# Kernel tuning notes

Measured on AMD Instinct MI355X. Metric: run time of the kernel, lower is better.

The kernel has to match this reference:

```python
import jax, jax.numpy as jnp
import numpy as np
import math

B, S, D, H, DQ, DV = 8, 1024, 1024, 16, 64, 64

def _layernorm(x, gamma, beta, eps=1e-5):
    mu = jnp.mean(x, axis=-1, keepdims=True)
    var = jnp.var(x, axis=-1, keepdims=True)
    return (x - mu) * jax.lax.rsqrt(var + eps) * gamma + beta

def setup_inputs() -> dict:
    key = jax.random.key(0)
    ks = jax.random.split(key, 6)
    x = jax.random.normal(ks[0], (B, S, D), dtype=jnp.float32)
    seq_lens = jax.random.randint(ks[1], (B,), 1, S + 1, dtype=jnp.int32)  # min 1 avoids fully-masked rows
    scale = 0.02
    Wq = jax.random.normal(ks[2], (D, H * DQ), dtype=jnp.float32) * scale
    Wkv = jax.random.normal(ks[3], (D, H * (DQ + DV)), dtype=jnp.float32) * scale
    Wo = jax.random.normal(ks[4], (H * DV, D), dtype=jnp.float32) * scale
    return {
        'x': x, 'seq_lens': seq_lens,
        'Wq': Wq, 'bq': jnp.zeros((H * DQ,), jnp.float32),
        'Wkv': Wkv, 'bkv': jnp.zeros((H * (DQ + DV),), jnp.float32),
        'Wo': Wo, 'bo': jnp.zeros((D,), jnp.float32),
        'gamma': jnp.ones((D,), jnp.float32), 'beta': jnp.zeros((D,), jnp.float32),
    }

def reference(x, seq_lens, Wq, bq, Wkv, bkv, Wo, bo, gamma, beta):
    # Decoder self-attention branch: query == key_value sequence.
    resid = x
    xn = _layernorm(x, gamma, beta)
    q = (xn @ Wq + bq).reshape(B, S, H, DQ).transpose(0, 2, 1, 3)      # bhqd
    kv = xn @ Wkv + bkv
    k = kv[..., : H * DQ].reshape(B, S, H, DQ).transpose(0, 2, 1, 3)   # bhkd
    v = kv[..., H * DQ :].reshape(B, S, H, DV).transpose(0, 2, 1, 3)   # bhkd
    scores = jnp.einsum('bhqd,bhkd->bhqk', q, k) / math.sqrt(DQ)
    key_pos = jnp.arange(S)
    pad_mask = key_pos[None, None, None, :] < seq_lens[:, None, None, None]  # [B,1,1,S]
    causal = jnp.tril(jnp.ones((S, S), dtype=bool))[None, None]              # [1,1,S,S]
    mask = pad_mask & causal
    scores = jnp.where(mask, scores, -jnp.inf)
    attn = jax.nn.softmax(scores, axis=-1)
    out = jnp.einsum('bhqk,bhkd->bhqd', attn, v)
    out = out.transpose(0, 2, 1, 3).reshape(B, S, H * DV)
    return out @ Wo + bo + resid
```

## Files before the change

### kernel.cpp

```cpp
#include <hip/hip_runtime.h>
#include <stdint.h>

#define ND 1024

typedef uint16_t u16;
typedef __bf16 bf16_t;
typedef bf16_t bf16x8 __attribute__((ext_vector_type(8)));
typedef float  f32x4  __attribute__((ext_vector_type(4)));
typedef u16    u16x8  __attribute__((ext_vector_type(8)));
typedef u16    u16x4  __attribute__((ext_vector_type(4)));

__device__ __forceinline__ float bf2f(u16 b){
    uint32_t u = ((uint32_t)b) << 16; float f; __builtin_memcpy(&f, &u, 4); return f;
}
__device__ __forceinline__ u16 f2bf(float f){
    uint32_t u; __builtin_memcpy(&u, &f, 4);
    u += 0x7FFFu + ((u >> 16) & 1u);
    return (u16)(u >> 16);
}
__device__ __forceinline__ bool bf_mode(const void* gamma){
    return *reinterpret_cast<const uint32_t*>(gamma) == 0x3F803F80u;
}
__device__ __forceinline__ float loadv(const void* p, int idx, bool bf){
    return bf ? bf2f(reinterpret_cast<const u16*>(p)[idx])
              : reinterpret_cast<const float*>(p)[idx];
}
__device__ __forceinline__ void gload16(const u16* g, u16* l){
    __builtin_amdgcn_global_load_lds(
        (const __attribute__((address_space(1))) void*)g,
        (__attribute__((address_space(3))) void*)l, 16, 0, 0);
}

__global__ __launch_bounds__(256) void k_ln(const void* __restrict__ x,
                                            const void* __restrict__ gamma,
                                            const void* __restrict__ beta,
                                            u16* __restrict__ xn){
    const bool bf = bf_mode(gamma);
    const int row = blockIdx.x;
    const int tid = threadIdx.x;
    const int base = row * ND + tid * 4;
    float v[4];
    if (bf){
        u16x4 t = *reinterpret_cast<const u16x4*>(reinterpret_cast<const u16*>(x) + base);
        #pragma unroll
        for (int e = 0; e < 4; e++) v[e] = bf2f(t[e]);
    } else {
        float4 t = *reinterpret_cast<const float4*>(reinterpret_cast<const float*>(x) + base);
        v[0] = t.x; v[1] = t.y; v[2] = t.z; v[3] = t.w;
    }
    float s1 = v[0] + v[1] + v[2] + v[3];
    float s2 = v[0]*v[0] + v[1]*v[1] + v[2]*v[2] + v[3]*v[3];
    #pragma unroll
    for (int off = 32; off; off >>= 1){
        s1 += __shfl_xor(s1, off);
        s2 += __shfl_xor(s2, off);
    }
    __shared__ float red1[4], red2[4];
    if ((tid & 63) == 0){ red1[tid >> 6] = s1; red2[tid >> 6] = s2; }
    __syncthreads();
    s1 = red1[0] + red1[1] + red1[2] + red1[3];
    s2 = red2[0] + red2[1] + red2[2] + red2[3];
    const float mu  = s1 * (1.0f / ND);
    const float var = s2 * (1.0f / ND) - mu * mu;
    const float rs  = rsqrtf(var + 1e-5f);
    u16x4 o;
    #pragma unroll
    for (int e = 0; e < 4; e++){
        float g = loadv(gamma, tid*4 + e, bf);
        float b = loadv(beta,  tid*4 + e, bf);
        o[e] = f2bf((v[e] - mu) * rs * g + b);
    }
    *reinterpret_cast<u16x4*>(xn + base) = o;
}

__global__ __launch_bounds__(256) void k_wt(const void* __restrict__ W,
                                            const void* __restrict__ gamma,
                                            u16* __restrict__ WT, int Ncols){
    const bool bf = bf_mode(gamma);
    __shared__ float tile[32][33];
    const int n0 = blockIdx.x * 32, k0 = blockIdx.y * 32;
    const int tx = threadIdx.x & 31, ty = threadIdx.x >> 5;
    #pragma unroll
    for (int r = 0; r < 4; r++){
        int kk = ty + r * 8;
        tile[kk][tx] = loadv(W, (k0 + kk) * Ncols + n0 + tx, bf);
    }
    __syncthreads();
    #pragma unroll
    for (int r = 0; r < 4; r++){
        int nn = ty + r * 8;
        WT[(size_t)(n0 + nn) * 1024 + k0 + tx] = f2bf(tile[tx][nn]);
    }
}

template<int MODE>
__global__ __launch_bounds__(256) void k_gemm(const u16* __restrict__ A,
                                              const u16* __restrict__ BT,
                                              const void* __restrict__ bias0,
                                              const void* __restrict__ bias1,
                                              const void* __restrict__ xres,
                                              const void* __restrict__ gamma,
                                              u16* __restrict__ Qo, u16* __restrict__ Ko,
                                              u16* __restrict__ Vo, float* __restrict__ outf){
    const bool bf = bf_mode(gamma);
    __shared__ u16 Al[128 * 64];
    __shared__ u16 Bl[128 * 64];
    const int bm = blockIdx.x & 63, bn = blockIdx.x >> 6;
    const int tid = threadIdx.x, lane = tid & 63, w = tid >> 6;
    const int wr = w >> 1, wc = w & 1;
    const int l15 = lane & 15, g = lane >> 4;
    const int xr = (l15 & 7) * 8;
    f32x4 acc[4][4];
    #pragma unroll
    for (int m = 0; m < 4; m++)
        #pragma unroll
        for (int n = 0; n < 4; n++) acc[m][n] = f32x4{0.f, 0.f, 0.f, 0.f};

    const u16* Ag = A  + (size_t)(bm * 128) * 1024;
    const u16* Bg = BT + (size_t)(bn * 128) * 1024;
    const int srow = tid >> 3, sslot = tid & 7;
    const int sswz = (sslot * 8) ^ ((srow & 7) * 8);

    for (int k0 = 0; k0 < 1024; k0 += 64){
        #pragma unroll
        for (int call = 0; call < 4; call++){
            const int row = srow + call * 32;
            const int c   = tid + call * 256;
            gload16(Ag + (size_t)row * 1024 + k0 + sswz, Al + c * 8);
            gload16(Bg + (size_t)row * 1024 + k0 + sswz, Bl + c * 8);
        }
        __syncthreads();
        #pragma unroll
        for (int kc = 0; kc < 2; kc++){
            bf16x8 af[4], bfr[4];
            #pragma unroll
            for (int m = 0; m < 4; m++){
                const int row = wr*64 + m*16 + l15;
                u16x8 t = *reinterpret_cast<const u16x8*>(&Al[row*64 + ((kc*32 + g*8) ^ xr)]);
                af[m] = __builtin_bit_cast(bf16x8, t);
            }
            #pragma unroll
            for (int n = 0; n < 4; n++){
                const int row = wc*64 + n*16 + l15;
                u16x8 t = *reinterpret_cast<const u16x8*>(&Bl[row*64 + ((kc*32 + g*8) ^ xr)]);
                bfr[n] = __builtin_bit_cast(bf16x8, t);
            }
            #pragma unroll
            for (int m = 0; m < 4; m++)
                #pragma unroll
                for (int n = 0; n < 4; n++)
                    acc[m][n] = __builtin_amdgcn_mfma_f32_16x16x32_bf16(af[m], bfr[n], acc[m][n], 0, 0, 0);
        }
        __syncthreads();
    }
    #pragma unroll
    for (int m = 0; m < 4; m++){
        const int grow = bm * 128 + wr * 64 + m * 16 + g * 4;
        #pragma unroll
        for (int n = 0; n < 4; n++){
            const int gcol = bn * 128 + wc * 64 + n * 16 + l15;
            #pragma unroll
            for (int r = 0; r < 4; r++){
                float val = acc[m][n][r];
                const int rr = grow + r;
                if (MODE == 0){
                    const int b = rr >> 10, s = rr & 1023;
                    if (gcol < 1024){
                        int h = gcol >> 6, d = gcol & 63;
                        val = (val + loadv(bias0, gcol, bf)) * 0.18033688011112042f;
                        Qo[((size_t)(b*16 + h) * 1024 + s) * 64 + d] = f2bf(val);
                    } else if (gcol < 2048){
                        int n2 = gcol - 1024, h = n2 >> 6, d = n2 & 63;
                        val += loadv(bias1, n2, bf);
                        Ko[((size_t)(b*16 + h) * 1024 + s) * 64 + d] = f2bf(val);
                    } else {
                        int n3 = gcol - 2048, h = n3 >> 6, d = n3 & 63;
                        val += loadv(bias1, gcol - 1024, bf);
                        Vo[((size_t)(b*16 + h) * 1024 + s) * 64 + d] = f2bf(val);
                    }
                } else {
                    val += loadv(bias0, gcol, bf);
                    val += loadv(xres, (int)((size_t)rr * 1024 + gcol), bf);
                    outf[(size_t)rr * 1024 + gcol] = val;
                }
            }
        }
    }
}

__global__ __launch_bounds__(64, 4) void k_attn(const u16* __restrict__ Q,
                                                const u16* __restrict__ K,
                                                const u16* __restrict__ V,
                                                const int* __restrict__ seq_lens,
                                                u16* __restrict__ AO){
    __shared__ u16 Kl0[32 * 64], Kl1[32 * 64];
    __shared__ u16 Vt[64 * 32];
    __shared__ u16 Pl[32 * 32];
    const int bid = blockIdx.x;
    const int qb = 31 - (bid >> 7);
    const int bh = bid & 127;
    const int b = bh >> 4, h = bh & 15;
    const int lane = threadIdx.x;
    const int l15 = lane & 15, g = lane >> 4;
    const int seqlen = seq_lens[b];
    const int nkt = (min(qb * 32 + 31, seqlen - 1) >> 5) + 1;
    const size_t kvbase = (size_t)bh * 1024;

    bf16x8 qa[2][2];
    #pragma unroll
    for (int m = 0; m < 2; m++)
        #pragma unroll
        for (int kc = 0; kc < 2; kc++){
            const u16* qp = Q + (kvbase + qb*32 + m*16 + l15) * 64 + kc*32 + g*8;
            qa[m][kc] = __builtin_bit_cast(bf16x8, *reinterpret_cast<const u16x8*>(qp));
        }

    float m_run[2] = {-3.0e38f, -3.0e38f};
    float l_run[2] = {0.f, 0.f};
    f32x4 oacc[2][4];
    #pragma unroll
    for (int m = 0; m < 2; m++)
        #pragma unroll
        for (int nf = 0; nf < 4; nf++) oacc[m][nf] = f32x4{0.f, 0.f, 0.f, 0.f};

    const int srow8 = lane >> 3, sslot = lane & 7;
    u16x8 vr[4];

    auto stageK = [&](int kt, u16* dst){
        #pragma unroll
        for (int call = 0; call < 4; call++){
            const int row = srow8 + call * 8;
            const int c   = lane + call * 64;
            gload16(K + (kvbase + kt*32 + row) * 64 + ((sslot * 8) ^ ((row & 7) * 8)), dst + c * 8);
        }
    };
    auto vload = [&](int kt){
        #pragma unroll
        for (int j = 0; j < 4; j++){
            const int c = lane + j * 64;
            vr[j] = *reinterpret_cast<const u16x8*>(V + (kvbase + kt*32 + (c >> 3)) * 64 + (c & 7) * 8);
        }
    };
    auto vstore = [&](){
        #pragma unroll
        for (int j = 0; j < 4; j++){
            const int c = lane + j * 64, k = c >> 3, sl = c & 7;
            #pragma unroll
            for (int i = 0; i < 8; i++){
                const int d = sl * 8 + i;
                Vt[d * 32 + (((k >> 3) ^ ((d >> 3) & 3)) * 8) + (k & 7)] = vr[j][i];
            }
        }
    };

    stageK(0, Kl0); vload(0);
    u16* kcur = Kl0; u16* knext = Kl1;

    for (int kt = 0; kt < nkt; kt++){
        asm volatile("s_waitcnt vmcnt(0)" ::: "memory");
        __builtin_amdgcn_sched_barrier(0);
        vstore();
        const bool pre = (kt + 1 < nkt);
        if (pre){ stageK(kt + 1, knext); vload(kt + 1); }

        f32x4 sa[2][2];
        #pragma unroll
        for (int m = 0; m < 2; m++)
            #pragma unroll
            for (int n = 0; n < 2; n++) sa[m][n] = f32x4{0.f, 0.f, 0.f, 0.f};
        #pragma unroll
        for (int kc = 0; kc < 2; kc++){
            bf16x8 kf[2];
            #pragma unroll
            for (int n = 0; n < 2; n++){
                const int row = n*16 + l15;
                u16x8 t = *reinterpret_cast<const u16x8*>(&kcur[row*64 + ((kc*32 + g*8) ^ ((l15 & 7) * 8))]);
                kf[n] = __builtin_bit_cast(bf16x8, t);
            }
            #pragma unroll
            for (int m = 0; m < 2; m++)
                #pragma unroll
                for (int n = 0; n < 2; n++)
                    sa[m][n] = __builtin_amdgcn_mfma_f32_16x16x32_bf16(kf[n], qa[m][kc], sa[m][n], 0, 0, 0);
        }

        #pragma unroll
        for (int m = 0; m < 2; m++){
            const int q = qb*32 + m*16 + l15;
            const int klim = min(q, seqlen - 1);
            float p[8];
            float rm = -3.0e38f;
            #pragma unroll
            for (int n = 0; n < 2; n++)
                #pragma unroll
                for (int r = 0; r < 4; r++){
                    const int k = kt*32 + n*16 + g*4 + r;
                    float sv = sa[m][n][r];
                    sv = (k <= klim) ? sv : -3.0e38f;
                    p[n*4 + r] = sv;
                    rm = fmaxf(rm, sv);
                }
            rm = fmaxf(rm, __shfl_xor(rm, 16));
            rm = fmaxf(rm, __shfl_xor(rm, 32));
            const float mnew = fmaxf(m_run[m], rm);
            const float fac  = exp2f(m_run[m] - mnew);
            m_run[m] = mnew;
            float rs = 0.f;
            #pragma unroll
            for (int n = 0; n < 2; n++)
                #pragma unroll
                for (int r = 0; r < 4; r++){
                    const float ev = exp2f(p[n*4 + r] - mnew);
                    rs += ev;
                    const int ql = m*16 + l15;
                    const int k  = n*16 + g*4 + r;
                    Pl[ql * 32 + (k ^ ((ql & 3) * 8))] = f2bf(ev);
                }
            rs += __shfl_xor(rs, 16);
            rs += __shfl_xor(rs, 32);
            l_run[m] = l_run[m] * fac + rs;
            #pragma unroll
            for (int r = 0; r < 4; r++){
                const float facr = __shfl(fac, g*4 + r, 16);
                #pragma unroll
                for (int nf = 0; nf < 4; nf++) oacc[m][nf][r] *= facr;
            }
        }

        {
            bf16x8 pa[2], vf[4];
            #pragma unroll
            for (int m = 0; m < 2; m++){
                const int ql = m*16 + l15;
                u16x8 t = *reinterpret_cast<const u16x8*>(&Pl[ql * 32 + ((g ^ (ql & 3)) * 8)]);
                pa[m] = __builtin_bit_cast(bf16x8, t);
            }
            #pragma unroll
            for (int nf = 0; nf < 4; nf++){
                const int dv = nf*16 + l15;
                u16x8 t = *reinterpret_cast<const u16x8*>(&Vt[dv * 32 + ((g ^ ((dv >> 3) & 3)) * 8)]);
                vf[nf] = __builtin_bit_cast(bf16x8, t);
            }
            #pragma unroll
            for (int m = 0; m < 2; m++)
                #pragma unroll
                for (int nf = 0; nf < 4; nf++)
                    oacc[m][nf] = __builtin_amdgcn_mfma_f32_16x16x32_bf16(pa[m], vf[nf], oacc[m][nf], 0, 0, 0);
        }
        u16* tmp = kcur; kcur = knext; knext = tmp;
    }

    #pragma unroll
    for (int m = 0; m < 2; m++)
        #pragma unroll
        for (int r = 0; r < 4; r++){
            const float lv  = __shfl(l_run[m], g*4 + r, 16);
            const float inv = 1.0f / lv;
            const int sg = qb*32 + m*16 + g*4 + r;
            #pragma unroll
            for (int nf = 0; nf < 4; nf++){
                const int col = h * 64 + nf * 16 + l15;
                AO[((size_t)b * 1024 + sg) * 1024 + col] = f2bf(oacc[m][nf][r] * inv);
            }
        }
}

extern "C" void kernel_launch(void* const* d_in, const int* in_sizes, int n_in,
                              void* d_out, int out_size, void* d_ws, size_t ws_size,
                              hipStream_t stream){
    const int exp_sizes[10] = {8388608, 8, 1048576, 1024, 2097152, 2048, 1048576, 1024, 1024, 1024};
    if (n_in != 10) return;
    for (int i = 0; i < 10; i++) if (in_sizes[i] != exp_sizes[i]) return;

    const void* x     = d_in[0];
    const int*  slen  = (const int*)d_in[1];
    const void* Wq    = d_in[2];
    const void* bq    = d_in[3];
    const void* Wkv   = d_in[4];
    const void* bkv   = d_in[5];
    const void* Wo    = d_in[6];
    const void* bo    = d_in[7];
    const void* gamma = d_in[8];
    const void* beta  = d_in[9];

    u16* WTqkv = (u16*)d_ws;
    u16* WoT   = WTqkv + (size_t)3072 * 1024;
    u16* xn    = WoT   + (size_t)1024 * 1024;
    u16* Qb    = xn    + (size_t)8192 * 1024;
    u16* Kb    = Qb    + (size_t)8192 * 1024;
    u16* Vb    = Kb    + (size_t)8192 * 1024;
    u16* AOb   = xn;
    const size_t need = ((size_t)3072 + 1024 + 4 * 8192) * 1024 * 2;
    if (ws_size < need) return;

    k_ln<<<8192, 256, 0, stream>>>(x, gamma, beta, xn);
    k_wt<<<dim3(32, 32), 256, 0, stream>>>(Wq,  gamma, WTqkv, 1024);
    k_wt<<<dim3(64, 32), 256, 0, stream>>>(Wkv, gamma, WTqkv + (size_t)1024 * 1024, 2048);
    k_wt<<<dim3(32, 32), 256, 0, stream>>>(Wo,  gamma, WoT, 1024);
    k_gemm<0><<<64 * 24, 256, 0, stream>>>(xn, WTqkv, bq, bkv, nullptr, gamma,
                                           Qb, Kb, Vb, nullptr);
    k_attn<<<4096, 64, 0, stream>>>(Qb, Kb, Vb, slen, AOb);
    k_gemm<1><<<64 * 8, 256, 0, stream>>>(AOb, WoT, bo, nullptr, x, gamma,
                                          nullptr, nullptr, nullptr, (float*)d_out);
}
```

Baseline: 230.9 us.

## Enlarge GEMM tiles to 256x256 with double-buffered LDS and XCD block remap

Both projection GEMMs move from 128x128 tiles with 256 threads to 256x256 tiles with 1024 threads (16 waves, each still computing a 64x64 sub-tile). The LDS staging is double-buffered so the next K-slice is loaded while the current one is computed, needing only one barrier per iteration. Block indices are remapped so consecutive tiles are spread across the eight XCDs, which is meant to improve L2 locality. The cost is far fewer workgroups: 384 for the QKV GEMM and 128 for the output GEMM, which can leave many CUs idle or create tail imbalance. The kernel also uses 128KB of LDS per block.

```diff
diff --git a/kernel.cpp b/kernel.cpp
--- a/kernel.cpp
+++ b/kernel.cpp
@@ -93,21 +93,23 @@
     }
 }
 
-template<int MODE>
-__global__ __launch_bounds__(256) void k_gemm(const u16* __restrict__ A,
-                                              const u16* __restrict__ BT,
-                                              const void* __restrict__ bias0,
-                                              const void* __restrict__ bias1,
-                                              const void* __restrict__ xres,
-                                              const void* __restrict__ gamma,
-                                              u16* __restrict__ Qo, u16* __restrict__ Ko,
-                                              u16* __restrict__ Vo, float* __restrict__ outf){
+template<int MODE, int NBN>
+__global__ __launch_bounds__(1024, 4) void k_gemm(const u16* __restrict__ A,
+                                                  const u16* __restrict__ BT,
+                                                  const void* __restrict__ bias0,
+                                                  const void* __restrict__ bias1,
+                                                  const void* __restrict__ xres,
+                                                  const void* __restrict__ gamma,
+                                                  u16* __restrict__ Qo, u16* __restrict__ Ko,
+                                                  u16* __restrict__ Vo, float* __restrict__ outf){
     const bool bf = bf_mode(gamma);
-    __shared__ u16 Al[128 * 64];
-    __shared__ u16 Bl[128 * 64];
-    const int bm = blockIdx.x & 63, bn = blockIdx.x >> 6;
+    __shared__ u16 Al0[256 * 64], Bl0[256 * 64];
+    __shared__ u16 Al1[256 * 64], Bl1[256 * 64];
+    const int nwg = gridDim.x, chunk = nwg >> 3;
+    const int orig = (blockIdx.x & 7) * chunk + (blockIdx.x >> 3);
+    const int bm = orig / NBN, bn = orig % NBN;
     const int tid = threadIdx.x, lane = tid & 63, w = tid >> 6;
-    const int wr = w >> 1, wc = w & 1;
+    const int wr = w >> 2, wc = w & 3;
     const int l15 = lane & 15, g = lane >> 4;
     const int xr = (l15 & 7) * 8;
     f32x4 acc[4][4];
@@ -116,33 +118,34 @@
         #pragma unroll
         for (int n = 0; n < 4; n++) acc[m][n] = f32x4{0.f, 0.f, 0.f, 0.f};
 
-    const u16* Ag = A  + (size_t)(bm * 128) * 1024;
-    const u16* Bg = BT + (size_t)(bn * 128) * 1024;
-    const int srow = tid >> 3, sslot = tid & 7;
-    const int sswz = (sslot * 8) ^ ((srow & 7) * 8);
-
-    for (int k0 = 0; k0 < 1024; k0 += 64){
-        #pragma unroll
-        for (int call = 0; call < 4; call++){
-            const int row = srow + call * 32;
-            const int c   = tid + call * 256;
-            gload16(Ag + (size_t)row * 1024 + k0 + sswz, Al + c * 8);
-            gload16(Bg + (size_t)row * 1024 + k0 + sswz, Bl + c * 8);
-        }
-        __syncthreads();
+    const u16* Ag = A  + (size_t)(bm * 256) * 1024;
+    const u16* Bg = BT + (size_t)(bn * 256) * 1024;
+    const int sswz = ((tid & 7) * 8) ^ (((tid >> 3) & 7) * 8);
+
+    auto stage = [&](int t, u16* Ad, u16* Bd){
+        const int k0 = t * 64;
+        #pragma unroll
+        for (int call = 0; call < 2; call++){
+            const int c = tid + call * 1024;
+            const int row = c >> 3;
+            gload16(Ag + (size_t)row * 1024 + k0 + sswz, Ad + c * 8);
+            gload16(Bg + (size_t)row * 1024 + k0 + sswz, Bd + c * 8);
+        }
+    };
+    auto compute = [&](const u16* Ac, const u16* Bc){
         #pragma unroll
         for (int kc = 0; kc < 2; kc++){
             bf16x8 af[4], bfr[4];
             #pragma unroll
             for (int m = 0; m < 4; m++){
                 const int row = wr*64 + m*16 + l15;
-                u16x8 t = *reinterpret_cast<const u16x8*>(&Al[row*64 + ((kc*32 + g*8) ^ xr)]);
+                u16x8 t = *reinterpret_cast<const u16x8*>(&Ac[row*64 + ((kc*32 + g*8) ^ xr)]);
                 af[m] = __builtin_bit_cast(bf16x8, t);
             }
             #pragma unroll
             for (int n = 0; n < 4; n++){
                 const int row = wc*64 + n*16 + l15;
-                u16x8 t = *reinterpret_cast<const u16x8*>(&Bl[row*64 + ((kc*32 + g*8) ^ xr)]);
+                u16x8 t = *reinterpret_cast<const u16x8*>(&Bc[row*64 + ((kc*32 + g*8) ^ xr)]);
                 bfr[n] = __builtin_bit_cast(bf16x8, t);
             }
             #pragma unroll
@@ -151,14 +154,24 @@
                 for (int n = 0; n < 4; n++)
                     acc[m][n] = __builtin_amdgcn_mfma_f32_16x16x32_bf16(af[m], bfr[n], acc[m][n], 0, 0, 0);
         }
+    };
+
+    stage(0, Al0, Bl0);
+    __syncthreads();
+    #pragma unroll 2
+    for (int t = 0; t < 16; t++){
+        const bool cur1 = (t & 1);
+        if (t + 1 < 16) stage(t + 1, cur1 ? Al0 : Al1, cur1 ? Bl0 : Bl1);
+        compute(cur1 ? Al1 : Al0, cur1 ? Bl1 : Bl0);
         __syncthreads();
     }
+
     #pragma unroll
     for (int m = 0; m < 4; m++){
-        const int grow = bm * 128 + wr * 64 + m * 16 + g * 4;
+        const int grow = bm * 256 + wr * 64 + m * 16 + g * 4;
         #pragma unroll
         for (int n = 0; n < 4; n++){
-            const int gcol = bn * 128 + wc * 64 + n * 16 + l15;
+            const int gcol = bn * 256 + wc * 64 + n * 16 + l15;
             #pragma unroll
             for (int r = 0; r < 4; r++){
                 float val = acc[m][n][r];
@@ -397,9 +410,9 @@
     k_wt<<<dim3(32, 32), 256, 0, stream>>>(Wq,  gamma, WTqkv, 1024);
     k_wt<<<dim3(64, 32), 256, 0, stream>>>(Wkv, gamma, WTqkv + (size_t)1024 * 1024, 2048);
     k_wt<<<dim3(32, 32), 256, 0, stream>>>(Wo,  gamma, WoT, 1024);
-    k_gemm<0><<<64 * 24, 256, 0, stream>>>(xn, WTqkv, bq, bkv, nullptr, gamma,
-                                           Qb, Kb, Vb, nullptr);
+    k_gemm<0, 12><<<384, 1024, 0, stream>>>(xn, WTqkv, bq, bkv, nullptr, gamma,
+                                            Qb, Kb, Vb, nullptr);
     k_attn<<<4096, 64, 0, stream>>>(Qb, Kb, Vb, slen, AOb);
-    k_gemm<1><<<64 * 8, 256, 0, stream>>>(AOb, WoT, bo, nullptr, x, gamma,
-                                          nullptr, nullptr, nullptr, (float*)d_out);
-}
+    k_gemm<1, 4><<<128, 1024, 0, stream>>>(AOb, WoT, bo, nullptr, x, gamma,
+                                           nullptr, nullptr, nullptr, (float*)d_out);
+}
```

Result: slower. 258.6 us (+12.0%).

## Use 256x256 eight-wave pipelined GEMM for QKV and one-wave-per-row LayerNorm

Applied to the files above, without the earlier changes.

Replaces the 128x128 QKV projection GEMM with a 512-thread, 256x256-tile kernel. It double-buffers the A and B halves in LDS with direct global-to-LDS loads and interleaves those loads with MFMA quads behind barriers and setprio hints. Blocks are remapped across XCDs so neighbouring tiles share cache. LayerNorm now gives each row to one wave so it no longer needs the shared-memory reduction and block barrier. The bigger tile means more operand reuse per load, but only 384 blocks launch and each uses a lot of LDS, so occupancy and load balance across CUs may suffer.

```diff
diff --git a/kernel.cpp b/kernel.cpp
--- a/kernel.cpp
+++ b/kernel.cpp
@@ -36,41 +36,47 @@
                                             const void* __restrict__ beta,
                                             u16* __restrict__ xn){
     const bool bf = bf_mode(gamma);
-    const int row = blockIdx.x;
-    const int tid = threadIdx.x;
-    const int base = row * ND + tid * 4;
-    float v[4];
+    const int lane = threadIdx.x & 63;
+    const int row  = blockIdx.x * 4 + (threadIdx.x >> 6);
+    const size_t base = (size_t)row * 1024;
+    float v[16];
     if (bf){
-        u16x4 t = *reinterpret_cast<const u16x4*>(reinterpret_cast<const u16*>(x) + base);
-        #pragma unroll
-        for (int e = 0; e < 4; e++) v[e] = bf2f(t[e]);
+        const u16* xp = reinterpret_cast<const u16*>(x) + base;
+        #pragma unroll
+        for (int j = 0; j < 4; j++){
+            u16x4 t4 = *reinterpret_cast<const u16x4*>(xp + j*256 + lane*4);
+            #pragma unroll
+            for (int e = 0; e < 4; e++) v[j*4 + e] = bf2f(t4[e]);
+        }
     } else {
-        float4 t = *reinterpret_cast<const float4*>(reinterpret_cast<const float*>(x) + base);
-        v[0] = t.x; v[1] = t.y; v[2] = t.z; v[3] = t.w;
-    }
-    float s1 = v[0] + v[1] + v[2] + v[3];
-    float s2 = v[0]*v[0] + v[1]*v[1] + v[2]*v[2] + v[3]*v[3];
+        const float* xp = reinterpret_cast<const float*>(x) + base;
+        #pragma unroll
+        for (int j = 0; j < 4; j++){
+            float4 t = *reinterpret_cast<const float4*>(xp + j*256 + lane*4);
+            v[j*4+0] = t.x; v[j*4+1] = t.y; v[j*4+2] = t.z; v[j*4+3] = t.w;
+        }
+    }
+    float s1 = 0.f, s2 = 0.f;
+    #pragma unroll
+    for (int e = 0; e < 16; e++){ s1 += v[e]; s2 += v[e]*v[e]; }
     #pragma unroll
     for (int off = 32; off; off >>= 1){
         s1 += __shfl_xor(s1, off);
         s2 += __shfl_xor(s2, off);
     }
-    __shared__ float red1[4], red2[4];
-    if ((tid & 63) == 0){ red1[tid >> 6] = s1; red2[tid >> 6] = s2; }
-    __syncthreads();
-    s1 = red1[0] + red1[1] + red1[2] + red1[3];
-    s2 = red2[0] + red2[1] + red2[2] + red2[3];
     const float mu  = s1 * (1.0f / ND);
     const float var = s2 * (1.0f / ND) - mu * mu;
     const float rs  = rsqrtf(var + 1e-5f);
-    u16x4 o;
-    #pragma unroll
-    for (int e = 0; e < 4; e++){
-        float g = loadv(gamma, tid*4 + e, bf);
-        float b = loadv(beta,  tid*4 + e, bf);
-        o[e] = f2bf((v[e] - mu) * rs * g + b);
-    }
-    *reinterpret_cast<u16x4*>(xn + base) = o;
+    #pragma unroll
+    for (int j = 0; j < 4; j++){
+        u16x4 o;
+        #pragma unroll
+        for (int e = 0; e < 4; e++){
+            const int col = j*256 + lane*4 + e;
+            o[e] = f2bf((v[j*4+e] - mu) * rs * loadv(gamma, col, bf) + loadv(beta, col, bf));
+        }
+        *reinterpret_cast<u16x4*>(xn + base + j*256 + lane*4) = o;
+    }
 }
 
 __global__ __launch_bounds__(256) void k_wt(const void* __restrict__ W,
@@ -93,15 +99,155 @@
     }
 }
 
-template<int MODE>
-__global__ __launch_bounds__(256) void k_gemm(const u16* __restrict__ A,
-                                              const u16* __restrict__ BT,
-                                              const void* __restrict__ bias0,
-                                              const void* __restrict__ bias1,
-                                              const void* __restrict__ xres,
-                                              const void* __restrict__ gamma,
-                                              u16* __restrict__ Qo, u16* __restrict__ Ko,
-                                              u16* __restrict__ Vo, float* __restrict__ outf){
+__global__ __launch_bounds__(512, 2) void k_gemm8(const u16* __restrict__ A,
+                                                  const u16* __restrict__ BT,
+                                                  const void* __restrict__ bias0,
+                                                  const void* __restrict__ bias1,
+                                                  const void* __restrict__ gamma,
+                                                  u16* __restrict__ Qo, u16* __restrict__ Ko,
+                                                  u16* __restrict__ Vo){
+    __shared__ u16 Ah[2][2][128 * 64];
+    __shared__ u16 Bh[2][2][128 * 64];
+    const bool bf = bf_mode(gamma);
+    const int orig = (blockIdx.x & 7) * 48 + (blockIdx.x >> 3);
+    const int bm = orig / 12, bn = orig % 12;
+    const int tid = threadIdx.x, lane = tid & 63, w = tid >> 6;
+    const int wr = w >> 2, wc = w & 3;
+    const int l15 = lane & 15, g = lane >> 4;
+    f32x4 acc[8][4];
+    #pragma unroll
+    for (int m = 0; m < 8; m++)
+        #pragma unroll
+        for (int n = 0; n < 4; n++) acc[m][n] = f32x4{0.f, 0.f, 0.f, 0.f};
+
+    const u16* Ag = A  + (size_t)(bm * 256) * 1024;
+    const u16* Bg = BT + (size_t)(bn * 256) * 1024;
+
+    auto stA = [&](int kt, int h){
+        #pragma unroll
+        for (int j = 0; j < 2; j++){
+            const int c = tid + j * 512, row = c >> 3, sl = c & 7;
+            gload16(Ag + (size_t)(h * 128 + row) * 1024 + kt * 64 + ((sl ^ (row & 7)) * 8),
+                    &Ah[kt & 1][h][c * 8]);
+        }
+    };
+    auto stB = [&](int kt, int h){
+        #pragma unroll
+        for (int j = 0; j < 2; j++){
+            const int c = tid + j * 512, row = c >> 3, sl = c & 7;
+            gload16(Bg + (size_t)(h * 128 + row) * 1024 + kt * 64 + ((sl ^ (row & 7)) * 8),
+                    &Bh[kt & 1][h][c * 8]);
+        }
+    };
+    auto dsA = [&](int pk, int mm, int kc) -> bf16x8 {
+        const int rh = mm * 16 + l15;
+        u16x8 x8 = *reinterpret_cast<const u16x8*>(
+            &Ah[pk][wr][rh * 64 + (((kc * 4 + g) ^ (rh & 7)) * 8)]);
+        return __builtin_bit_cast(bf16x8, x8);
+    };
+    auto dsB = [&](int pk, int nn, int kc) -> bf16x8 {
+        const int rh = (wc & 1) * 64 + nn * 16 + l15;
+        u16x8 x8 = *reinterpret_cast<const u16x8*>(
+            &Bh[pk][wc >> 1][rh * 64 + (((kc * 4 + g) ^ (rh & 7)) * 8)]);
+        return __builtin_bit_cast(bf16x8, x8);
+    };
+    bf16x8 a0[2][2], b0[4][2];
+    auto quad = [&](int mq){
+        __builtin_amdgcn_s_setprio(1);
+        #pragma unroll
+        for (int kc = 0; kc < 2; kc++)
+            #pragma unroll
+            for (int mm = 0; mm < 2; mm++)
+                #pragma unroll
+                for (int n = 0; n < 4; n++)
+                    acc[mq * 2 + mm][n] = __builtin_amdgcn_mfma_f32_16x16x32_bf16(
+                        a0[mm][kc], b0[n][kc], acc[mq * 2 + mm][n], 0, 0, 0);
+        __builtin_amdgcn_s_setprio(0);
+    };
+    #define BAR() __builtin_amdgcn_s_barrier()
+
+    stA(0, 0); stA(0, 1); stB(0, 0); stB(0, 1); stB(1, 0); stB(1, 1);
+    asm volatile("s_waitcnt vmcnt(0)" ::: "memory");
+    BAR();
+
+    for (int t = 0; t < 8; t++){
+        const int k1 = 2 * t + 1, k2 = 2 * t + 2, k3 = 2 * t + 3;
+        const bool st = (t < 7);
+        #pragma unroll
+        for (int n = 0; n < 4; n++){ b0[n][0] = dsB(0, n, 0); b0[n][1] = dsB(0, n, 1); }
+        a0[0][0] = dsA(0, 0, 0); a0[0][1] = dsA(0, 0, 1);
+        a0[1][0] = dsA(0, 1, 0); a0[1][1] = dsA(0, 1, 1);
+        stA(k1, 0);
+        BAR(); quad(0); BAR();
+        a0[0][0] = dsA(0, 2, 0); a0[0][1] = dsA(0, 2, 1);
+        a0[1][0] = dsA(0, 3, 0); a0[1][1] = dsA(0, 3, 1);
+        stA(k1, 1);
+        BAR(); quad(1); BAR();
+        a0[0][0] = dsA(0, 4, 0); a0[0][1] = dsA(0, 4, 1);
+        a0[1][0] = dsA(0, 5, 0); a0[1][1] = dsA(0, 5, 1);
+        if (st) stB(k2, 0);
+        BAR(); quad(2); BAR();
+        a0[0][0] = dsA(0, 6, 0); a0[0][1] = dsA(0, 6, 1);
+        a0[1][0] = dsA(0, 7, 0); a0[1][1] = dsA(0, 7, 1);
+        if (st){ stB(k2, 1); asm volatile("s_waitcnt vmcnt(4)" ::: "memory"); }
+        else   { asm volatile("s_waitcnt vmcnt(0)" ::: "memory"); }
+        BAR(); quad(3); BAR();
+        #pragma unroll
+        for (int n = 0; n < 4; n++){ b0[n][0] = dsB(1, n, 0); b0[n][1] = dsB(1, n, 1); }
+        a0[0][0] = dsA(1, 0, 0); a0[0][1] = dsA(1, 0, 1);
+        a0[1][0] = dsA(1, 1, 0); a0[1][1] = dsA(1, 1, 1);
+        if (st) stA(k2, 0);
+        BAR(); quad(0); BAR();
+        a0[0][0] = dsA(1, 2, 0); a0[0][1] = dsA(1, 2, 1);
+        a0[1][0] = dsA(1, 3, 0); a0[1][1] = dsA(1, 3, 1);
+        if (st) stA(k2, 1);
+        BAR(); quad(1); BAR();
+        a0[0][0] = dsA(1, 4, 0); a0[0][1] = dsA(1, 4, 1);
+        a0[1][0] = dsA(1, 5, 0); a0[1][1] = dsA(1, 5, 1);
+        if (st) stB(k3, 0);
+        BAR(); quad(2); BAR();
+        a0[0][0] = dsA(1, 6, 0); a0[0][1] = dsA(1, 6, 1);
+        a0[1][0] = dsA(1, 7, 0); a0[1][1] = dsA(1, 7, 1);
+        if (st){ stB(k3, 1); asm volatile("s_waitcnt vmcnt(4)" ::: "memory"); }
+        BAR(); quad(3); BAR();
+    }
+    #undef BAR
+
+    #pragma unroll
+    for (int m = 0; m < 8; m++){
+        const int grow = bm * 256 + wr * 128 + m * 16 + g * 4;
+        #pragma unroll
+        for (int n = 0; n < 4; n++){
+            const int gcol = bn * 256 + wc * 64 + n * 16 + l15;
+            #pragma unroll
+            for (int r = 0; r < 4; r++){
+                float val = acc[m][n][r];
+                const int rr = grow + r;
+                const int b = rr >> 10, s = rr & 1023;
+                if (gcol < 1024){
+                    int h = gcol >> 6, d = gcol & 63;
+                    val = (val + loadv(bias0, gcol, bf)) * 0.18033688011112042f;
+                    Qo[((size_t)(b*16 + h) * 1024 + s) * 64 + d] = f2bf(val);
+                } else if (gcol < 2048){
+                    int n2 = gcol - 1024, h = n2 >> 6, d = n2 & 63;
+                    val += loadv(bias1, n2, bf);
+                    Ko[((size_t)(b*16 + h) * 1024 + s) * 64 + d] = f2bf(val);
+                } else {
+                    int n3 = gcol - 2048, h = n3 >> 6, d = n3 & 63;
+                    val += loadv(bias1, gcol - 1024, bf);
+                    Vo[((size_t)(b*16 + h) * 1024 + s) * 64 + d] = f2bf(val);
+                }
+            }
+        }
+    }
+}
+
+__global__ __launch_bounds__(256) void k_gemmB(const u16* __restrict__ A,
+                                               const u16* __restrict__ BT,
+                                               const void* __restrict__ bias0,
+                                               const void* __restrict__ xres,
+                                               const void* __restrict__ gamma,
+                                               float* __restrict__ outf){
     const bool bf = bf_mode(gamma);
     __shared__ u16 Al[128 * 64];
     __shared__ u16 Bl[128 * 64];
@@ -163,26 +309,9 @@
             for (int r = 0; r < 4; r++){
                 float val = acc[m][n][r];
                 const int rr = grow + r;
-                if (MODE == 0){
-                    const int b = rr >> 10, s = rr & 1023;
-                    if (gcol < 1024){
-                        int h = gcol >> 6, d = gcol & 63;
-                        val = (val + loadv(bias0, gcol, bf)) * 0.18033688011112042f;
-                        Qo[((size_t)(b*16 + h) * 1024 + s) * 64 + d] = f2bf(val);
-                    } else if (gcol < 2048){
-                        int n2 = gcol - 1024, h = n2 >> 6, d = n2 & 63;
-                        val += loadv(bias1, n2, bf);
-                        Ko[((size_t)(b*16 + h) * 1024 + s) * 64 + d] = f2bf(val);
-                    } else {
-                        int n3 = gcol - 2048, h = n3 >> 6, d = n3 & 63;
-                        val += loadv(bias1, gcol - 1024, bf);
-                        Vo[((size_t)(b*16 + h) * 1024 + s) * 64 + d] = f2bf(val);
-                    }
-                } else {
-                    val += loadv(bias0, gcol, bf);
-                    val += loadv(xres, (int)((size_t)rr * 1024 + gcol), bf);
-                    outf[(size_t)rr * 1024 + gcol] = val;
-                }
+                val += loadv(bias0, gcol, bf);
+                val += loadv(xres, (int)((size_t)rr * 1024 + gcol), bf);
+                outf[(size_t)rr * 1024 + gcol] = val;
             }
         }
     }
@@ -393,13 +522,11 @@
     const size_t need = ((size_t)3072 + 1024 + 4 * 8192) * 1024 * 2;
     if (ws_size < need) return;
 
-    k_ln<<<8192, 256, 0, stream>>>(x, gamma, beta, xn);
+    k_ln<<<2048, 256, 0, stream>>>(x, gamma, beta, xn);
     k_wt<<<dim3(32, 32), 256, 0, stream>>>(Wq,  gamma, WTqkv, 1024);
     k_wt<<<dim3(64, 32), 256, 0, stream>>>(Wkv, gamma, WTqkv + (size_t)1024 * 1024, 2048);
     k_wt<<<dim3(32, 32), 256, 0, stream>>>(Wo,  gamma, WoT, 1024);
-    k_gemm<0><<<64 * 24, 256, 0, stream>>>(xn, WTqkv, bq, bkv, nullptr, gamma,
-                                           Qb, Kb, Vb, nullptr);
+    k_gemm8<<<384, 512, 0, stream>>>(xn, WTqkv, bq, bkv, gamma, Qb, Kb, Vb);
     k_attn<<<4096, 64, 0, stream>>>(Qb, Kb, Vb, slen, AOb);
-    k_gemm<1><<<64 * 8, 256, 0, stream>>>(AOb, WoT, bo, nullptr, x, gamma,
-                                          nullptr, nullptr, nullptr, (float*)d_out);
-}
+    k_gemmB<<<512, 256, 0, stream>>>(AOb, WoT, bo, x, gamma, (float*)d_out);
+}
```

New measurement: 251.7 us. 1.09x slower.
